# Optimization experiments

Hardware: AMD Instinct MI355X
Metric: run time of the kernel (lower is better)

Reference implementation:

```python
import jax, jax.numpy as jnp
import numpy as np

D = 2048      # model_dim
H = 16        # num_heads
HD = D // H   # head_dim = 128
RQ = 512; RK = 512; RV = 512
B, T = 2, 2048


def setup_inputs() -> dict:
    key = jax.random.key(0)
    ks = jax.random.split(key, 9)
    s = lambda fan_in: 1.0 / np.sqrt(fan_in)
    return {
        "x":    jax.random.normal(ks[0], (B, T, D), dtype=jnp.float32),
        # nn.Linear weights stored [out, in]
        "wq_a": jax.random.uniform(ks[1], (RQ, D), jnp.float32, -s(D), s(D)),
        "wq_b": jax.random.uniform(ks[2], (H * HD, RQ), jnp.float32, -s(RQ), s(RQ)),
        "wk_a": jax.random.uniform(ks[3], (RK, D), jnp.float32, -s(D), s(D)),
        "wk_b": jax.random.uniform(ks[4], (H * HD, RK), jnp.float32, -s(RK), s(RK)),
        "wv_a": jax.random.uniform(ks[5], (RV, D), jnp.float32, -s(D), s(D)),
        "wv_b": jax.random.uniform(ks[6], (H * HD, RV), jnp.float32, -s(RV), s(RV)),
        "wo_w": jax.random.uniform(ks[7], (D, H * HD), jnp.float32, -s(H * HD), s(H * HD)),
        "wo_b": jax.random.uniform(ks[8], (D,), jnp.float32, -s(H * HD), s(H * HD)),
    }


def reference(x, wq_a, wq_b, wk_a, wk_b, wv_a, wv_b, wo_w, wo_b):
    b, t, d = x.shape
    # low-rank latent projections
    c_q = jnp.einsum('btd,rd->btr', x, wq_a)   # [b,t,RQ]
    c_k = jnp.einsum('btd,rd->btr', x, wk_a)   # [b,t,RK]
    c_v = jnp.einsum('btd,rd->btr', x, wv_a)   # [b,t,RV]
    # up-project and split heads: [b,h,t,hd]
    q = jnp.einsum('btr,er->bte', c_q, wq_b).reshape(b, t, H, HD).transpose(0, 2, 1, 3)
    k = jnp.einsum('btr,er->bte', c_k, wk_b).reshape(b, t, H, HD).transpose(0, 2, 1, 3)
    v = jnp.einsum('btr,er->bte', c_v, wv_b).reshape(b, t, H, HD).transpose(0, 2, 1, 3)
    # scaled dot-product attention (mask=None, dropout=0)
    scores = jnp.einsum('bhqd,bhkd->bhqk', q, k) / jnp.sqrt(jnp.float32(HD))
    attn = jax.nn.softmax(scores, axis=-1)
    out = jnp.einsum('bhqk,bhkd->bhqd', attn, v)
    out = out.transpose(0, 2, 1, 3).reshape(b, t, d)
    return jnp.einsum('bte,de->btd', out, wo_w) + wo_b
```

## Files before the change

kernel.cpp:

```cpp
#include <hip/hip_runtime.h>

typedef __attribute__((ext_vector_type(8))) short short8;
typedef __attribute__((ext_vector_type(4))) float f32x4;
typedef __attribute__((ext_vector_type(4))) float float4v;
typedef __attribute__((ext_vector_type(4))) unsigned short us4;

__device__ __forceinline__ unsigned short f2bf(float f) {
  union { float f; unsigned int u; } c; c.f = f;
  unsigned int u = c.u;
  u += 0x7fffu + ((u >> 16) & 1u);
  return (unsigned short)(u >> 16);
}

__device__ __forceinline__ unsigned int pkbf(float a, float b) {
  unsigned int r;
  asm("v_cvt_pk_bf16_f32 %0, %1, %2" : "=v"(r) : "v"(a), "v"(b));
  return r;
}

__device__ __forceinline__ float exp2r(float x) {
#if __has_builtin(__builtin_amdgcn_exp2f)
  return __builtin_amdgcn_exp2f(x);
#else
  return exp2f(x);
#endif
}

__device__ __forceinline__ void async16(const void* g, void* l) {
  __builtin_amdgcn_global_load_lds(
      (const __attribute__((address_space(1))) unsigned int*)g,
      (__attribute__((address_space(3))) unsigned int*)l, 16, 0, 0);
}

__device__ __forceinline__ f32x4 mfma16(short8 a, short8 b, f32x4 c) {
  return __builtin_amdgcn_mfma_f32_16x16x32_bf16(a, b, c, 0, 0, 0);
}

__global__ void cast_all(const float* __restrict__ x,
                         const float* __restrict__ wqa, const float* __restrict__ wqb,
                         const float* __restrict__ wka, const float* __restrict__ wkb,
                         const float* __restrict__ wva, const float* __restrict__ wvb,
                         const float* __restrict__ wow,
                         unsigned short* __restrict__ out) {
  int c = blockIdx.x * 256 + threadIdx.x;
  const int stride = gridDim.x * 256;
  for (; c < 4718592; c += stride) {
    int i = c << 2;
    const float* src; int off;
    if (i < 8388608)       { src = x;   off = 0; }
    else if (i < 9437184)  { src = wqa; off = 8388608; }
    else if (i < 10485760) { src = wka; off = 9437184; }
    else if (i < 11534336) { src = wva; off = 10485760; }
    else if (i < 12582912) { src = wqb; off = 11534336; }
    else if (i < 13631488) { src = wkb; off = 12582912; }
    else if (i < 14680064) { src = wvb; off = 13631488; }
    else                   { src = wow; off = 14680064; }
    float4v v = *(const float4v*)(src + (i - off));
    us4 r;
    r[0] = f2bf(v[0]); r[1] = f2bf(v[1]); r[2] = f2bf(v[2]); r[3] = f2bf(v[3]);
    *(us4*)(out + i) = r;
  }
}

template <int BN>
__device__ __forceinline__ void gemm_body(
    const unsigned short* __restrict__ A, int lda,
    const unsigned short* __restrict__ B, int ldb,
    void* __restrict__ Cv, int ldc,
    const float* __restrict__ bias, float qscale, int K, int mode) {
  constexpr int NT = BN / 32;
  __shared__ __align__(16) unsigned short As[128 * 64];
  __shared__ __align__(16) unsigned short Bs[BN * 64];
  const int tid  = threadIdx.x;
  const int wave = tid >> 6, lane = tid & 63;
  const int lr = lane & 15, lg = lane >> 4;
  const int lr7 = lr & 7;
  const int tile_m = blockIdx.y << 7;
  const int tile_n = blockIdx.x * BN;
  const int wm = (wave & 1) << 6;
  const int wn = (wave >> 1) * (BN / 2);

  f32x4 acc[4][NT];
#pragma unroll
  for (int i = 0; i < 4; i++)
#pragma unroll
    for (int j = 0; j < NT; j++) acc[i][j] = (f32x4)0.0f;

  const int srow = tid >> 3;
  const int cg = ((tid & 7) ^ (srow & 7)) << 3;
  const unsigned short* Ag = A + (size_t)(tile_m + srow) * lda + cg;
  const unsigned short* Bg = B + (size_t)(tile_n + srow) * ldb + cg;
  const size_t rowskipA = (size_t)32 * lda;
  const size_t rowskipB = (size_t)32 * ldb;
  unsigned short* AsW = As + wave * 512;
  unsigned short* BsW = Bs + wave * 512;

  for (int k0 = 0; k0 < K; k0 += 64) {
#pragma unroll
    for (int i = 0; i < 4; i++)
      async16(Ag + k0 + i * rowskipA, AsW + i * 2048);
#pragma unroll
    for (int i = 0; i < BN / 32; i++)
      async16(Bg + k0 + i * rowskipB, BsW + i * 2048);
    __syncthreads();
#pragma unroll
    for (int kk = 0; kk < 2; kk++) {
      short8 af[4], bf[NT];
#pragma unroll
      for (int mt = 0; mt < 4; mt++)
        af[mt] = *(const short8*)&As[(wm + mt * 16 + lr) * 64 + (((kk * 4 + lg) ^ lr7) << 3)];
#pragma unroll
      for (int nt = 0; nt < NT; nt++)
        bf[nt] = *(const short8*)&Bs[(wn + nt * 16 + lr) * 64 + (((kk * 4 + lg) ^ lr7) << 3)];
#pragma unroll
      for (int mt = 0; mt < 4; mt++)
#pragma unroll
        for (int nt = 0; nt < NT; nt++)
          acc[mt][nt] = mfma16(af[mt], bf[nt], acc[mt][nt]);
    }
    __syncthreads();
  }

#pragma unroll
  for (int mt = 0; mt < 4; mt++) {
#pragma unroll
    for (int nt = 0; nt < NT; nt++) {
#pragma unroll
      for (int r = 0; r < 4; r++) {
        int row = tile_m + wm + mt * 16 + lg * 4 + r;
        int col = tile_n + wn + nt * 16 + lr;
        float v = acc[mt][nt][r];
        if (mode == 0) {
          ((unsigned short*)Cv)[(size_t)row * ldc + col] = f2bf(v);
        } else if (mode == 3) {
          ((unsigned short*)Cv)[(size_t)row * ldc + col] = f2bf(v * qscale);
        } else if (mode == 1) {
          int tl = row & 2047;
          int key = tl & 63;
          int tp = (tl & ~63) | ((key & 15) << 2) | (key >> 4);
          ((unsigned short*)Cv)[((size_t)((row >> 11) << 11) + col) * 2048 + tp] = f2bf(v);
        } else {
          ((float*)Cv)[(size_t)row * ldc + col] = v + bias[col];
        }
      }
    }
  }
}

__global__ __launch_bounds__(256)
void gemm_k128(const unsigned short* __restrict__ A, int lda,
               const unsigned short* __restrict__ B, int ldb,
               void* __restrict__ C, int ldc, const float* __restrict__ bias,
               int K, int mode) {
  gemm_body<128>(A, lda, B, ldb, C, ldc, bias, 1.0f, K, mode);
}

__global__ __launch_bounds__(256)
void gemm_k64(const unsigned short* __restrict__ A, int lda,
              const unsigned short* __restrict__ B, int ldb,
              void* __restrict__ C, int ldc, const float* __restrict__ bias,
              int K, int mode) {
  gemm_body<64>(A, lda, B, ldb, C, ldc, bias, 1.0f, K, mode);
}

__global__ __launch_bounds__(256)
void gemm_up(const unsigned short* __restrict__ cdown,
             const unsigned short* __restrict__ wup,
             unsigned short* __restrict__ qb,
             unsigned short* __restrict__ kb,
             unsigned short* __restrict__ vtb) {
  const int z = blockIdx.z;
  const unsigned short* A = cdown + z * 512;
  const unsigned short* B = wup + (size_t)z * 1048576;
  void* C; int mode; float qs = 1.0f;
  if (z == 0)      { C = qb;  mode = 3; qs = 0.12751744f; }
  else if (z == 1) { C = kb;  mode = 0; }
  else             { C = vtb; mode = 1; }
  gemm_body<128>(A, 1536, B, 512, C, 2048, nullptr, qs, 512, mode);
}

__global__ __launch_bounds__(512)
void attn(const unsigned short* __restrict__ q,
          const unsigned short* __restrict__ k,
          const unsigned short* __restrict__ vt,
          unsigned short* __restrict__ o) {
  __shared__ __align__(16) unsigned short Ks[2][64 * 128];
  __shared__ __align__(16) unsigned short Vs[2][128 * 64];
  __shared__ __align__(16) unsigned short Ps[8][16 * 64];

  const int tid  = threadIdx.x;
  const int wave = tid >> 6, lane = tid & 63;
  const int lr = lane & 15, lg = lane >> 4;
  const int lin = blockIdx.x + (blockIdx.y << 4);
  const int xcd = lin & 7;
  const int lcl = lin >> 3;
  const int bh = (xcd << 2) | (lcl & 3);
  const int b = bh >> 4, h = bh & 15;
  const int q0 = (lcl >> 2) << 7;

  const size_t qrow = (size_t)(b * 2048 + q0 + wave * 16 + lr);
  short8 qf[4];
#pragma unroll
  for (int kk = 0; kk < 4; kk++)
    qf[kk] = *(const short8*)(q + qrow * 2048 + h * 128 + kk * 32 + lg * 8);

  f32x4 oacc[8];
  f32x4 lacc = (f32x4)0.0f;
#pragma unroll
  for (int n2 = 0; n2 < 8; n2++) oacc[n2] = (f32x4)0.0f;

  short8 ones;
#pragma unroll
  for (int j = 0; j < 8; j++) ones[j] = (short)0x3F80;

  const unsigned short* kg = k  + (size_t)(b * 2048 + (tid >> 4)) * 2048 + h * 128
                               + ((((tid & 15) ^ (tid >> 4)) & 15) << 3);
  const unsigned short* vg = vt + (size_t)(bh * 128 + (tid >> 3)) * 2048
                               + (((tid & 7) ^ ((tid >> 3) & 7)) << 3);
  const int lr7 = lr & 7;

#pragma unroll
  for (int i = 0; i < 2; i++) {
    async16(kg + (size_t)(i * 32) * 2048, &Ks[0][i * 4096 + wave * 512]);
    async16(vg + (size_t)(i * 64) * 2048, &Vs[0][i * 4096 + wave * 512]);
    async16(kg + (size_t)(64 + i * 32) * 2048, &Ks[1][i * 4096 + wave * 512]);
  }
  __syncthreads();

  short8 pfA, pfB;
  {
    f32x4 sv[4];
#pragma unroll
    for (int nt = 0; nt < 4; nt++) sv[nt] = (f32x4)0.0f;
#pragma unroll
    for (int nt = 0; nt < 4; nt++) {
#pragma unroll
      for (int kk = 0; kk < 4; kk++) {
        short8 kf = *(const short8*)&Ks[0][(nt * 16 + lr) * 128 + (((kk * 4 + lg) ^ lr) << 3)];
        sv[nt] = mfma16(qf[kk], kf, sv[nt]);
      }
    }
#pragma unroll
    for (int r = 0; r < 4; r++) {
      float p0 = exp2r(sv[0][r]);
      float p1 = exp2r(sv[1][r]);
      float p2 = exp2r(sv[2][r]);
      float p3 = exp2r(sv[3][r]);
      uint2 pk; pk.x = pkbf(p0, p1); pk.y = pkbf(p2, p3);
      int row = lg * 4 + r;
      *(uint2*)&Ps[wave][row * 64 + ((lr ^ (lg << 2)) << 2)] = pk;
    }
    pfA = *(const short8*)&Ps[wave][lr * 64 + (((lg * 2) ^ ((lr >> 2) << 2)) << 2)];
    pfB = *(const short8*)&Ps[wave][lr * 64 + (((8 + lg * 2) ^ ((lr >> 2) << 2)) << 2)];
  }
  __syncthreads();

  for (int t = 0; t < 31; ++t) {
    const int buf = t & 1;
    if (t < 30) {
#pragma unroll
      for (int i = 0; i < 2; i++)
        async16(kg + (size_t)((t + 2) * 64 + i * 32) * 2048, &Ks[buf][i * 4096 + wave * 512]);
    }
#pragma unroll
    for (int i = 0; i < 2; i++)
      async16(vg + (t + 1) * 64 + (size_t)(i * 64) * 2048, &Vs[buf ^ 1][i * 4096 + wave * 512]);

    const unsigned short* KsN = Ks[buf ^ 1];
    const unsigned short* VsB = Vs[buf];

    __builtin_amdgcn_s_setprio(1);
    f32x4 sv[4];
#pragma unroll
    for (int nt = 0; nt < 4; nt++) sv[nt] = (f32x4)0.0f;
#pragma unroll
    for (int nt = 0; nt < 4; nt++) {
#pragma unroll
      for (int kk = 0; kk < 4; kk++) {
        short8 kf = *(const short8*)&KsN[(nt * 16 + lr) * 128 + (((kk * 4 + lg) ^ lr) << 3)];
        sv[nt] = mfma16(qf[kk], kf, sv[nt]);
      }
    }

    lacc = mfma16(pfA, ones, lacc);
#pragma unroll
    for (int n2 = 0; n2 < 8; n2++) {
      short8 vf = *(const short8*)&VsB[(n2 * 16 + lr) * 64 + ((lg ^ lr7) << 3)];
      oacc[n2] = mfma16(pfA, vf, oacc[n2]);
    }
    lacc = mfma16(pfB, ones, lacc);
#pragma unroll
    for (int n2 = 0; n2 < 8; n2++) {
      short8 vf = *(const short8*)&VsB[(n2 * 16 + lr) * 64 + (((4 + lg) ^ lr7) << 3)];
      oacc[n2] = mfma16(pfB, vf, oacc[n2]);
    }
    __builtin_amdgcn_s_setprio(0);

#pragma unroll
    for (int r = 0; r < 4; r++) {
      float p0 = exp2r(sv[0][r]);
      float p1 = exp2r(sv[1][r]);
      float p2 = exp2r(sv[2][r]);
      float p3 = exp2r(sv[3][r]);
      uint2 pk; pk.x = pkbf(p0, p1); pk.y = pkbf(p2, p3);
      int row = lg * 4 + r;
      *(uint2*)&Ps[wave][row * 64 + ((lr ^ (lg << 2)) << 2)] = pk;
    }
    pfA = *(const short8*)&Ps[wave][lr * 64 + (((lg * 2) ^ ((lr >> 2) << 2)) << 2)];
    pfB = *(const short8*)&Ps[wave][lr * 64 + (((8 + lg * 2) ^ ((lr >> 2) << 2)) << 2)];

    __syncthreads();
  }

  {
    const unsigned short* VsB = Vs[1];
    __builtin_amdgcn_s_setprio(1);
    lacc = mfma16(pfA, ones, lacc);
#pragma unroll
    for (int n2 = 0; n2 < 8; n2++) {
      short8 vf = *(const short8*)&VsB[(n2 * 16 + lr) * 64 + ((lg ^ lr7) << 3)];
      oacc[n2] = mfma16(pfA, vf, oacc[n2]);
    }
    lacc = mfma16(pfB, ones, lacc);
#pragma unroll
    for (int n2 = 0; n2 < 8; n2++) {
      short8 vf = *(const short8*)&VsB[(n2 * 16 + lr) * 64 + (((4 + lg) ^ lr7) << 3)];
      oacc[n2] = mfma16(pfB, vf, oacc[n2]);
    }
    __builtin_amdgcn_s_setprio(0);
  }

  f32x4 inv;
#pragma unroll
  for (int r = 0; r < 4; r++) inv[r] = 1.0f / lacc[r];
#pragma unroll
  for (int n2 = 0; n2 < 8; n2++)
#pragma unroll
    for (int r = 0; r < 4; r++) {
      size_t row = (size_t)(b * 2048 + q0 + wave * 16 + lg * 4 + r);
      o[row * 2048 + h * 128 + n2 * 16 + lr] = f2bf(oacc[n2][r] * inv[r]);
    }
}

extern "C" void kernel_launch(void* const* d_in, const int* in_sizes, int n_in,
                              void* d_out, int out_size, void* d_ws, size_t ws_size,
                              hipStream_t stream) {
  const float* x    = (const float*)d_in[0];
  const float* wq_a = (const float*)d_in[1];
  const float* wq_b = (const float*)d_in[2];
  const float* wk_a = (const float*)d_in[3];
  const float* wk_b = (const float*)d_in[4];
  const float* wv_a = (const float*)d_in[5];
  const float* wv_b = (const float*)d_in[6];
  const float* wo_w = (const float*)d_in[7];
  const float* wo_b = (const float*)d_in[8];
  float* out = (float*)d_out;

  unsigned short* ws = (unsigned short*)d_ws;
  unsigned short* xb    = ws;
  unsigned short* wdown = ws + 8388608;
  unsigned short* wupb  = ws + 11534336;
  unsigned short* wow   = ws + 14680064;
  unsigned short* cdown = ws + 18874368;
  unsigned short* qb    = ws + 25165824;
  unsigned short* kb    = ws + 33554432;
  unsigned short* vtb   = ws + 41943040;
  unsigned short* ao    = ws + 50331648;

  cast_all<<<dim3(2048), dim3(256), 0, stream>>>(x, wq_a, wq_b, wk_a, wk_b, wv_a, wv_b, wo_w, ws);

  gemm_k64<<<dim3(24, 32), dim3(256), 0, stream>>>(xb, 2048, wdown, 2048, cdown, 1536, nullptr, 2048, 0);

  gemm_up<<<dim3(16, 32, 3), dim3(256), 0, stream>>>(cdown, wupb, qb, kb, vtb);

  attn<<<dim3(16, 32), dim3(512), 0, stream>>>(qb, kb, vtb, ao);

  gemm_k64<<<dim3(32, 32), dim3(256), 0, stream>>>(ao, 2048, wow, 2048, out, 2048, wo_b, 2048, 2);
}
```

Baseline: 347.9 us.

## Double-buffer LDS in down/out GEMMs and remap blocks per XCD

Adds a double-buffered GEMM body that issues async global-to-LDS loads for the next K-step while computing the current one, which removes one barrier per iteration. The down-projection and output GEMMs now use it, launched on 1D grids whose block indices are remapped so that each XCD works on a contiguous group of N tiles for better L2 reuse. The cost is twice the LDS per block, which may reduce occupancy. The up-projection and attention kernels are unchanged.

```diff
diff --git a/kernel.cpp b/kernel.cpp
--- a/kernel.cpp
+++ b/kernel.cpp
@@ -62,6 +62,37 @@
   }
 }
 
+template <int NT>
+__device__ __forceinline__ void gemm_epilogue(
+    f32x4 (&acc)[4][NT], void* __restrict__ Cv, int ldc,
+    const float* __restrict__ bias, float qscale, int mode,
+    int tile_m, int tile_n, int wm, int wn, int lr, int lg) {
+#pragma unroll
+  for (int mt = 0; mt < 4; mt++) {
+#pragma unroll
+    for (int nt = 0; nt < NT; nt++) {
+#pragma unroll
+      for (int r = 0; r < 4; r++) {
+        int row = tile_m + wm + mt * 16 + lg * 4 + r;
+        int col = tile_n + wn + nt * 16 + lr;
+        float v = acc[mt][nt][r];
+        if (mode == 0) {
+          ((unsigned short*)Cv)[(size_t)row * ldc + col] = f2bf(v);
+        } else if (mode == 3) {
+          ((unsigned short*)Cv)[(size_t)row * ldc + col] = f2bf(v * qscale);
+        } else if (mode == 1) {
+          int tl = row & 2047;
+          int key = tl & 63;
+          int tp = (tl & ~63) | ((key & 15) << 2) | (key >> 4);
+          ((unsigned short*)Cv)[((size_t)((row >> 11) << 11) + col) * 2048 + tp] = f2bf(v);
+        } else {
+          ((float*)Cv)[(size_t)row * ldc + col] = v + bias[col];
+        }
+      }
+    }
+  }
+}
+
 template <int BN>
 __device__ __forceinline__ void gemm_body(
     const unsigned short* __restrict__ A, int lda,
@@ -120,47 +151,100 @@
     }
     __syncthreads();
   }
-
-#pragma unroll
-  for (int mt = 0; mt < 4; mt++) {
-#pragma unroll
-    for (int nt = 0; nt < NT; nt++) {
-#pragma unroll
-      for (int r = 0; r < 4; r++) {
-        int row = tile_m + wm + mt * 16 + lg * 4 + r;
-        int col = tile_n + wn + nt * 16 + lr;
-        float v = acc[mt][nt][r];
-        if (mode == 0) {
-          ((unsigned short*)Cv)[(size_t)row * ldc + col] = f2bf(v);
-        } else if (mode == 3) {
-          ((unsigned short*)Cv)[(size_t)row * ldc + col] = f2bf(v * qscale);
-        } else if (mode == 1) {
-          int tl = row & 2047;
-          int key = tl & 63;
-          int tp = (tl & ~63) | ((key & 15) << 2) | (key >> 4);
-          ((unsigned short*)Cv)[((size_t)((row >> 11) << 11) + col) * 2048 + tp] = f2bf(v);
-        } else {
-          ((float*)Cv)[(size_t)row * ldc + col] = v + bias[col];
-        }
-      }
-    }
-  }
+  gemm_epilogue<NT>(acc, Cv, ldc, bias, qscale, mode, tile_m, tile_n, wm, wn, lr, lg);
+}
+
+template <int BN>
+__device__ __forceinline__ void gemm_body_db(
+    const unsigned short* __restrict__ A, int lda,
+    const unsigned short* __restrict__ B, int ldb,
+    void* __restrict__ Cv, int ldc,
+    const float* __restrict__ bias, float qscale, int K, int mode,
+    int tile_m, int tile_n) {
+  constexpr int NT = BN / 32;
+  __shared__ __align__(16) unsigned short As[2][128 * 64];
+  __shared__ __align__(16) unsigned short Bs[2][BN * 64];
+  const int tid  = threadIdx.x;
+  const int wave = tid >> 6, lane = tid & 63;
+  const int lr = lane & 15, lg = lane >> 4;
+  const int lr7 = lr & 7;
+  const int wm = (wave & 1) << 6;
+  const int wn = (wave >> 1) * (BN / 2);
+
+  f32x4 acc[4][NT];
+#pragma unroll
+  for (int i = 0; i < 4; i++)
+#pragma unroll
+    for (int j = 0; j < NT; j++) acc[i][j] = (f32x4)0.0f;
+
+  const int srow = tid >> 3;
+  const int cg = ((tid & 7) ^ (srow & 7)) << 3;
+  const unsigned short* Ag = A + (size_t)(tile_m + srow) * lda + cg;
+  const unsigned short* Bg = B + (size_t)(tile_n + srow) * ldb + cg;
+  const size_t rowskipA = (size_t)32 * lda;
+  const size_t rowskipB = (size_t)32 * ldb;
+  const int woff = wave * 512;
+
+#pragma unroll
+  for (int i = 0; i < 4; i++)
+    async16(Ag + i * rowskipA, &As[0][woff + i * 2048]);
+#pragma unroll
+  for (int i = 0; i < BN / 32; i++)
+    async16(Bg + i * rowskipB, &Bs[0][woff + i * 2048]);
+  __syncthreads();
+
+  const int nsteps = K >> 6;
+  for (int s = 0; s < nsteps; ++s) {
+    const int buf = s & 1;
+    if (s + 1 < nsteps) {
+      const int k0 = (s + 1) << 6;
+#pragma unroll
+      for (int i = 0; i < 4; i++)
+        async16(Ag + k0 + i * rowskipA, &As[buf ^ 1][woff + i * 2048]);
+#pragma unroll
+      for (int i = 0; i < BN / 32; i++)
+        async16(Bg + k0 + i * rowskipB, &Bs[buf ^ 1][woff + i * 2048]);
+    }
+#pragma unroll
+    for (int kk = 0; kk < 2; kk++) {
+      short8 af[4], bf[NT];
+#pragma unroll
+      for (int mt = 0; mt < 4; mt++)
+        af[mt] = *(const short8*)&As[buf][(wm + mt * 16 + lr) * 64 + (((kk * 4 + lg) ^ lr7) << 3)];
+#pragma unroll
+      for (int nt = 0; nt < NT; nt++)
+        bf[nt] = *(const short8*)&Bs[buf][(wn + nt * 16 + lr) * 64 + (((kk * 4 + lg) ^ lr7) << 3)];
+#pragma unroll
+      for (int mt = 0; mt < 4; mt++)
+#pragma unroll
+        for (int nt = 0; nt < NT; nt++)
+          acc[mt][nt] = mfma16(af[mt], bf[nt], acc[mt][nt]);
+    }
+    __syncthreads();
+  }
+  gemm_epilogue<NT>(acc, Cv, ldc, bias, qscale, mode, tile_m, tile_n, wm, wn, lr, lg);
 }
 
 __global__ __launch_bounds__(256)
-void gemm_k128(const unsigned short* __restrict__ A, int lda,
-               const unsigned short* __restrict__ B, int ldb,
-               void* __restrict__ C, int ldc, const float* __restrict__ bias,
-               int K, int mode) {
-  gemm_body<128>(A, lda, B, ldb, C, ldc, bias, 1.0f, K, mode);
+void gemm_dn(const unsigned short* __restrict__ A,
+             const unsigned short* __restrict__ B,
+             unsigned short* __restrict__ C) {
+  const int lin = blockIdx.x;
+  const int xcd = lin & 7, l = lin >> 3;
+  const int tn = (xcd * 3 + l % 3) << 6;
+  const int tm = (l / 3) << 7;
+  gemm_body_db<64>(A, 2048, B, 2048, C, 1536, nullptr, 1.0f, 2048, 0, tm, tn);
 }
 
 __global__ __launch_bounds__(256)
-void gemm_k64(const unsigned short* __restrict__ A, int lda,
-              const unsigned short* __restrict__ B, int ldb,
-              void* __restrict__ C, int ldc, const float* __restrict__ bias,
-              int K, int mode) {
-  gemm_body<64>(A, lda, B, ldb, C, ldc, bias, 1.0f, K, mode);
+void gemm_out(const unsigned short* __restrict__ A,
+              const unsigned short* __restrict__ B,
+              float* __restrict__ C, const float* __restrict__ bias) {
+  const int lin = blockIdx.x;
+  const int xcd = lin & 7, l = lin >> 3;
+  const int tn = ((xcd << 2) + (l & 3)) << 6;
+  const int tm = (l >> 2) << 7;
+  gemm_body_db<64>(A, 2048, B, 2048, C, 2048, bias, 1.0f, 2048, 2, tm, tn);
 }
 
 __global__ __launch_bounds__(256)
@@ -369,11 +453,11 @@
 
   cast_all<<<dim3(2048), dim3(256), 0, stream>>>(x, wq_a, wq_b, wk_a, wk_b, wv_a, wv_b, wo_w, ws);
 
-  gemm_k64<<<dim3(24, 32), dim3(256), 0, stream>>>(xb, 2048, wdown, 2048, cdown, 1536, nullptr, 2048, 0);
+  gemm_dn<<<dim3(768), dim3(256), 0, stream>>>(xb, wdown, cdown);
 
   gemm_up<<<dim3(16, 32, 3), dim3(256), 0, stream>>>(cdown, wupb, qb, kb, vtb);
 
   attn<<<dim3(16, 32), dim3(512), 0, stream>>>(qb, kb, vtb, ao);
 
-  gemm_k64<<<dim3(32, 32), dim3(256), 0, stream>>>(ao, 2048, wow, 2048, out, 2048, wo_b, 2048, 2);
-}
+  gemm_out<<<dim3(1024), dim3(256), 0, stream>>>(ao, wow, out, wo_b);
+}
```

After: 381.8 us. +9.8%, slower.
